# Kernel optimization log

Hardware: AMD Instinct MI355X
Metric: run time of the kernel (lower is better)

Reference implementation:

```python
import jax, jax.numpy as jnp
import numpy as np

B, S, D, H = 2, 2048, 256, 8
W_STD = 0.02


def setup_inputs() -> dict:
    key = jax.random.key(0)
    ks = jax.random.split(key, 6)
    x = jax.random.normal(ks[0], (B, S, D), jnp.float32)
    e = jax.random.normal(ks[1], (B, S, D), jnp.float32)
    p = jax.random.normal(ks[2], (B, S, D), jnp.float32)
    W_q = W_STD * jax.random.normal(ks[3], (D, D), jnp.float32)
    W_k = W_STD * jax.random.normal(ks[4], (D, D), jnp.float32)
    W_v = W_STD * jax.random.normal(ks[5], (D, D), jnp.float32)
    gamma = jnp.ones((H, 1, 1), jnp.float32)
    return {"x": x, "e": e, "p": p, "W_q": W_q, "W_k": W_k, "W_v": W_v, "gamma": gamma}


def reference(x, e, p, W_q, W_k, W_v, gamma):
    # use_ppe=True: Q = K = p (broadcast to every head), V = e; each head sees
    # the SAME d_embed-wide copy, so project once and broadcast over heads.
    Q = p @ W_q  # [B,S,D]
    K = p @ W_k  # [B,S,D]
    V = e @ W_v  # [B,S,D]
    # squared euclidean distance (torch.cdist(...,p=2)**2), shared across heads
    q2 = jnp.sum(Q * Q, axis=-1)  # [B,S]
    k2 = jnp.sum(K * K, axis=-1)  # [B,S]
    d2 = q2[:, :, None] + k2[:, None, :] - 2.0 * jnp.einsum('bsd,btd->bst', Q, K)
    d2 = jnp.maximum(d2, 0.0)  # [B,S,S]
    # rbf kernel, per-head gamma: krn = exp(-d2 / (-2*gamma + 1e-6))
    krn = -d2[:, None, :, :] / (-2.0 * gamma + 1e-6)  # [B,H,S,S]
    causal = jnp.tril(jnp.ones((S, S), dtype=bool))  # True where attending allowed
    krn = jnp.where(causal, krn, -jnp.inf)
    krn = jnp.exp(krn)  # masked entries -> exp(-inf) = 0
    # dropout layers run in eval mode (identity)
    out = jnp.einsum('bhst,btd->bhsd', krn, V)  # [B,H,S,D]
    return out
```

## Files before the change

### kernel.cpp

```cpp
#include <hip/hip_runtime.h>
#include <hip/hip_bf16.h>


#define BB   2
#define SS   2048
#define DD   256
#define HH   8
#define BSR  (BB*SS)
#define TSPLIT 4

typedef __bf16 bf16_t;
typedef __bf16 bf16x8 __attribute__((ext_vector_type(8)));
typedef float  f32x4  __attribute__((ext_vector_type(4)));

static __device__ __forceinline__ f32x4 mfma16(bf16x8 a, bf16x8 b, f32x4 c) {
    return __builtin_amdgcn_mfma_f32_16x16x32_bf16(a, b, c, 0, 0, 0);
}

__global__ __launch_bounds__(256) void att_wtrans(
    const float* __restrict__ Wq, const float* __restrict__ Wk,
    const float* __restrict__ Wv,
    bf16_t* __restrict__ WFq_h, bf16_t* __restrict__ WFq_l,
    bf16_t* __restrict__ WFk_h, bf16_t* __restrict__ WFk_l,
    bf16_t* __restrict__ WFv, float* __restrict__ q2, float* __restrict__ k2)
{
    __shared__ float tT[64][68];
    const int tid = threadIdx.x;
    if (blockIdx.x == 48) {
        for (int i = tid; i < BSR; i += 256) { q2[i] = 0.f; k2[i] = 0.f; }
        return;
    }
    const int mat = blockIdx.x >> 4;
    const int tl  = blockIdx.x & 15;
    const int tr  = (tl >> 2) * 64, tc = (tl & 3) * 64;
    const float* W = (mat == 0) ? Wq : ((mat == 1) ? Wk : Wv);

#pragma unroll
    for (int i = 0; i < 4; ++i) {
        const int fidx = i * 256 + tid;
        const int r  = fidx >> 4;
        const int c4 = fidx & 15;
        const float4 v = *(const float4*)(W + (size_t)(tr + r) * DD + tc + c4 * 4);
        tT[c4 * 4 + 0][r] = v.x; tT[c4 * 4 + 1][r] = v.y;
        tT[c4 * 4 + 2][r] = v.z; tT[c4 * 4 + 3][r] = v.w;
    }
    __syncthreads();

#pragma unroll
    for (int i = 0; i < 2; ++i) {
        const int uidx  = i * 256 + tid;
        const int chunk = uidx >> 6;
        const int kc_l  = chunk >> 2, c16 = chunk & 3;
        const int u = uidx & 63, m16 = u & 15, quad = u >> 4;
        const float* src = &tT[c16 * 16 + m16][kc_l * 32 + quad * 8];
        const float4 a = *(const float4*)src;
        const float4 bq = *(const float4*)(src + 4);
        const float f[8] = {a.x, a.y, a.z, a.w, bq.x, bq.y, bq.z, bq.w};
        bf16x8 hi, lo;
#pragma unroll
        for (int j = 0; j < 8; ++j) {
            const bf16_t h = (bf16_t)f[j];
            hi[j] = h; lo[j] = (bf16_t)(f[j] - (float)h);
        }
        const int g16 = (tc >> 4) + c16;
        const int kcg = (tr >> 5) + kc_l;
        const size_t off = ((size_t)(g16 * 8 + kcg)) * 512 + (size_t)u * 8;
        if (mat == 0)      { *(bf16x8*)(WFq_h + off) = hi; *(bf16x8*)(WFq_l + off) = lo; }
        else if (mat == 1) { *(bf16x8*)(WFk_h + off) = hi; *(bf16x8*)(WFk_l + off) = lo; }
        else               { *(bf16x8*)(WFv + off)  = hi; }
    }
}

__global__ __launch_bounds__(256) void att_zero_reps(
    const float* __restrict__ gamma, float* __restrict__ out)
{
    const int h = blockIdx.y & (HH - 1);
    const int b = blockIdx.y / HH;
    int rep = 0;
    while (gamma[rep] != gamma[h]) ++rep;
    if (rep != h) return;
    float4* dst = (float4*)(out + ((size_t)b * HH + h) * SS * DD);
    const int n4 = SS * DD / 4;
    for (int i = blockIdx.x * 256 + threadIdx.x; i < n4; i += 64 * 256)
        dst[i] = float4{0.f, 0.f, 0.f, 0.f};
}

__global__ __launch_bounds__(256, 2) void att_gemm_qkv(
    const float* __restrict__ p, const float* __restrict__ e,
    const bf16_t* __restrict__ WFq_h, const bf16_t* __restrict__ WFq_l,
    const bf16_t* __restrict__ WFk_h, const bf16_t* __restrict__ WFk_l,
    const bf16_t* __restrict__ WFv,
    bf16_t* __restrict__ Qh, bf16_t* __restrict__ Ql,
    bf16_t* __restrict__ Kh, bf16_t* __restrict__ Kl,
    bf16_t* __restrict__ Vt, float* __restrict__ q2, float* __restrict__ k2)
{
    __shared__ float pL[16][264];
    __shared__ float eL[16][264];
    __shared__ bf16_t vts[64][16];

    const int tid  = threadIdx.x;
    const int w    = tid >> 6;
    const int lane = tid & 63;
    const int m16  = lane & 15;
    const int quad = lane >> 4;
    const int row0 = (blockIdx.x >> 2) * 16;
    const int nb   = blockIdx.x & 3;
    const int ncol = nb * 64 + w * 16 + m16;

#pragma unroll
    for (int i = 0; i < 4; ++i) {
        const int fidx = i * 256 + tid;
        const int r  = fidx >> 6;
        const int c4 = fidx & 63;
        const float4 pv = *(const float4*)(p + (size_t)(row0 + r) * DD + c4 * 4);
        const float4 ev = *(const float4*)(e + (size_t)(row0 + r) * DD + c4 * 4);
        *(float4*)&pL[r][c4 * 4] = pv;
        *(float4*)&eL[r][c4 * 4] = ev;
    }
    __syncthreads();

    f32x4 aQ = f32x4{0.f, 0.f, 0.f, 0.f};
    f32x4 aK = f32x4{0.f, 0.f, 0.f, 0.f};
    f32x4 aV = f32x4{0.f, 0.f, 0.f, 0.f};

#pragma unroll 2
    for (int kc = 0; kc < 8; ++kc) {
        const float* ps = &pL[m16][kc * 32 + quad * 8];
        const float* es = &eL[m16][kc * 32 + quad * 8];
        const float4 p0 = *(const float4*)ps;
        const float4 p1 = *(const float4*)(ps + 4);
        const float4 e0 = *(const float4*)es;
        const float4 e1 = *(const float4*)(es + 4);
        const float pa[8] = {p0.x, p0.y, p0.z, p0.w, p1.x, p1.y, p1.z, p1.w};
        const float ea[8] = {e0.x, e0.y, e0.z, e0.w, e1.x, e1.y, e1.z, e1.w};
        bf16x8 aph, apl, aeb;
#pragma unroll
        for (int j = 0; j < 8; ++j) {
            const bf16_t h = (bf16_t)pa[j];
            aph[j] = h;
            apl[j] = (bf16_t)(pa[j] - (float)h);
            aeb[j] = (bf16_t)ea[j];
        }
        const size_t wo = ((size_t)((nb * 4 + w) * 8 + kc)) * 512 + (size_t)lane * 8;
        const bf16x8 bqh = *(const bf16x8*)(WFq_h + wo);
        const bf16x8 bql = *(const bf16x8*)(WFq_l + wo);
        const bf16x8 bkh = *(const bf16x8*)(WFk_h + wo);
        const bf16x8 bkl = *(const bf16x8*)(WFk_l + wo);
        const bf16x8 bv  = *(const bf16x8*)(WFv + wo);
        aQ = mfma16(aph, bqh, aQ);
        aQ = mfma16(apl, bqh, aQ);
        aQ = mfma16(aph, bql, aQ);
        aK = mfma16(aph, bkh, aK);
        aK = mfma16(apl, bkh, aK);
        aK = mfma16(aph, bkl, aK);
        aV = mfma16(aeb, bv, aV);
    }

    float sq[4], sk[4];
#pragma unroll
    for (int r = 0; r < 4; ++r) {
        const int rl = quad * 4 + r;
        const size_t go = (size_t)(row0 + rl) * DD + ncol;
        const float qv = aQ[r], kv = aK[r], vv = aV[r];
        const bf16_t qh_ = (bf16_t)qv; const bf16_t ql_ = (bf16_t)(qv - (float)qh_);
        const bf16_t kh_ = (bf16_t)kv; const bf16_t kl_ = (bf16_t)(kv - (float)kh_);
        Qh[go] = qh_; Ql[go] = ql_;
        Kh[go] = kh_; Kl[go] = kl_;
        sq[r] = qv * qv; sk[r] = kv * kv;
        vts[w * 16 + m16][rl] = (bf16_t)vv;
    }

#pragma unroll
    for (int r = 0; r < 4; ++r) {
        float vq = sq[r], vk = sk[r];
#pragma unroll
        for (int off = 8; off >= 1; off >>= 1) {
            vq += __shfl_xor(vq, off);
            vk += __shfl_xor(vk, off);
        }
        if (m16 == 0) {
            atomicAdd(q2 + row0 + quad * 4 + r, vq);
            atomicAdd(k2 + row0 + quad * 4 + r, vk);
        }
    }

    __syncthreads();
    if (tid < 64) {
        const int bb2 = row0 >> 11, t0v = row0 & 2047;
        bf16_t* dst = Vt + ((size_t)bb2 * DD + nb * 64 + tid) * SS + t0v;
        *(uint4*)dst       = *(const uint4*)&vts[tid][0];
        *((uint4*)dst + 1) = *(const uint4*)&vts[tid][8];
    }
}

__global__ __launch_bounds__(256) void att_repack(
    const bf16_t* __restrict__ Qh, const bf16_t* __restrict__ Ql,
    const bf16_t* __restrict__ Kh, const bf16_t* __restrict__ Kl,
    const bf16_t* __restrict__ Vt,
    bf16_t* __restrict__ QFh, bf16_t* __restrict__ QFl,
    bf16_t* __restrict__ KFh, bf16_t* __restrict__ KFl,
    bf16_t* __restrict__ VF)
{
    __shared__ bf16_t rowT[64][264];
    __shared__ bf16_t vT[256][72];

    const int tid  = threadIdx.x;
    const int tt   = blockIdx.x;
    const int part = blockIdx.y;
    const int b    = blockIdx.z;

    if (part < 4) {
        const bf16_t* src = (part == 0) ? Kh : (part == 1) ? Kl
                          : (part == 2) ? Qh : Ql;
#pragma unroll
        for (int i = 0; i < 8; ++i) {
            const int off = (i * 256 + tid) * 8;
            const int r = off >> 8, c = off & 255;
            *(bf16x8*)&rowT[r][c] =
                *(const bf16x8*)(src + ((size_t)(b * SS + tt * 64 + r)) * DD + c);
        }
        __syncthreads();
        if (part < 2) {
            bf16_t* dst = (part == 0) ? KFh : KFl;
#pragma unroll
            for (int i = 0; i < 8; ++i) {
                const int g = i * 256 + tid;
                const int chunk = g >> 6, u = g & 63;
                const int w_ = chunk >> 3, kc = chunk & 7;
                const bf16x8 v = *(const bf16x8*)
                    &rowT[w_ * 16 + (u & 15)][kc * 32 + (u >> 4) * 8];
                *(bf16x8*)(dst + ((size_t)(b * 32 + tt)) * 16384 + (size_t)g * 8) = v;
            }
        } else {
            bf16_t* dst = (part == 2) ? QFh : QFl;
#pragma unroll
            for (int i = 0; i < 8; ++i) {
                const int g = i * 256 + tid;
                const int chunk = g >> 6, u = g & 63;
                const int sub = chunk >> 4, mt = (chunk >> 3) & 1, kc = chunk & 7;
                const bf16x8 v = *(const bf16x8*)
                    &rowT[sub * 32 + mt * 16 + (u & 15)][kc * 32 + (u >> 4) * 8];
                const int st = tt * 2 + sub;
                *(bf16x8*)(dst + ((size_t)(b * 64 + st)) * 8192
                               + (size_t)(mt * 8 + kc) * 512 + (size_t)u * 8) = v;
            }
        }
    } else {
#pragma unroll
        for (int i = 0; i < 8; ++i) {
            const int off = (i * 256 + tid) * 8;
            const int d = off >> 6, tcol = off & 63;
            *(bf16x8*)&vT[d][tcol] =
                *(const bf16x8*)(Vt + ((size_t)(b * DD + d)) * SS + tt * 64 + tcol);
        }
        __syncthreads();
#pragma unroll
        for (int i = 0; i < 8; ++i) {
            const int g = i * 256 + tid;
            const int chunk = g >> 6, u = g & 63;
            const int w_ = chunk >> 3, kc2 = (chunk >> 2) & 1, nt = chunk & 3;
            const bf16x8 v = *(const bf16x8*)
                &vT[w_ * 64 + nt * 16 + (u & 15)][kc2 * 32 + (u >> 4) * 8];
            *(bf16x8*)(VF + ((size_t)(b * 32 + tt)) * 16384 + (size_t)g * 8) = v;
        }
    }
}

__global__ __launch_bounds__(256, 2) void att_flash(
    const bf16_t* __restrict__ QFh, const bf16_t* __restrict__ QFl,
    const bf16_t* __restrict__ KFh, const bf16_t* __restrict__ KFl,
    const bf16_t* __restrict__ VF, const float* __restrict__ q2,
    const float* __restrict__ k2, const float* __restrict__ gamma,
    float* __restrict__ out)
{
    __shared__ bf16_t Pb[2][32][72];

    const int tid   = threadIdx.x;
    const int pair  = blockIdx.x;
    const int split = blockIdx.y;
    const int b     = blockIdx.z;
    const int wave  = tid >> 6;
    const int lane  = tid & 63;
    const int m16   = lane & 15;
    const int quad  = lane >> 4;

    float g[8];
#pragma unroll
    for (int h = 0; h < 8; ++h) g[h] = gamma[h];

    int pb = 0;

    for (int half = 0; half < 2; ++half) {
        const int st = half ? (63 - pair) : pair;
        const int s0 = st * 32;

        bf16x8 aQh[2][8], aQl[2][8];
        const size_t qtile = ((size_t)(b * 64 + st)) * 8192 + (size_t)lane * 8;
#pragma unroll
        for (int mt = 0; mt < 2; ++mt)
#pragma unroll
            for (int kc = 0; kc < 8; ++kc) {
                const size_t base = qtile + (size_t)(mt * 8 + kc) * 512;
                aQh[mt][kc] = *(const bf16x8*)(QFh + base);
                aQl[mt][kc] = *(const bf16x8*)(QFl + base);
            }

        float q2r[2][4];
#pragma unroll
        for (int mt = 0; mt < 2; ++mt)
#pragma unroll
            for (int r = 0; r < 4; ++r)
                q2r[mt][r] = q2[b * SS + s0 + mt * 16 + quad * 4 + r];

        const int n_tiles = (s0 + 31) / 64 + 1;

        for (int h = 0; h < HH; ++h) {
            int rep = 0;
            while (g[rep] != g[h]) ++rep;
            if (rep != h) continue;
            const float cexp = 1.0f / (2.0f * g[h] - 1e-6f);

            f32x4 O[2][4];
#pragma unroll
            for (int mt = 0; mt < 2; ++mt)
#pragma unroll
                for (int nt = 0; nt < 4; ++nt)
                    O[mt][nt] = f32x4{0.f, 0.f, 0.f, 0.f};

            for (int ti = split; ti < n_tiles; ti += TSPLIT) {
                const int t0 = ti * 64;
                const int tg = t0 + wave * 16 + m16;
                const size_t tile = ((size_t)(b * 32 + ti)) * 16384
                                  + (size_t)wave * 4096 + (size_t)lane * 8;

                bf16x8 vf[2][4];
#pragma unroll
                for (int kc2 = 0; kc2 < 2; ++kc2)
#pragma unroll
                    for (int nt = 0; nt < 4; ++nt)
                        vf[kc2][nt] = *(const bf16x8*)(
                            VF + tile + (size_t)(kc2 * 4 + nt) * 512);
                const float k2v = k2[b * SS + tg];

                f32x4 acc0 = f32x4{0.f, 0.f, 0.f, 0.f};
                f32x4 acc1 = f32x4{0.f, 0.f, 0.f, 0.f};
#pragma unroll
                for (int kc = 0; kc < 8; ++kc) {
                    const bf16x8 bh = *(const bf16x8*)(KFh + tile + (size_t)kc * 512);
                    const bf16x8 bl = *(const bf16x8*)(KFl + tile + (size_t)kc * 512);
                    acc0 = mfma16(aQh[0][kc], bh, acc0);
                    acc1 = mfma16(aQh[1][kc], bh, acc1);
                    acc0 = mfma16(aQl[0][kc], bh, acc0);
                    acc1 = mfma16(aQl[1][kc], bh, acc1);
                    acc0 = mfma16(aQh[0][kc], bl, acc0);
                    acc1 = mfma16(aQh[1][kc], bl, acc1);
                }

#pragma unroll
                for (int mt = 0; mt < 2; ++mt) {
#pragma unroll
                    for (int r = 0; r < 4; ++r) {
                        const int sl = mt * 16 + quad * 4 + r;
                        const int sg = s0 + sl;
                        const float dotv = mt ? acc1[r] : acc0[r];
                        float d2 = q2r[mt][r] + k2v - 2.0f * dotv;
                        d2 = fmaxf(d2, 0.0f);
                        const float wgt = (tg <= sg) ? __expf(cexp * d2) : 0.0f;
                        Pb[pb][sl][wave * 16 + m16] = (bf16_t)wgt;
                    }
                }
                __syncthreads();

#pragma unroll
                for (int kc2 = 0; kc2 < 2; ++kc2) {
                    const bf16x8 pa0 = *(const bf16x8*)&Pb[pb][m16][kc2 * 32 + quad * 8];
                    const bf16x8 pa1 = *(const bf16x8*)&Pb[pb][m16 + 16][kc2 * 32 + quad * 8];
#pragma unroll
                    for (int nt = 0; nt < 4; ++nt) {
                        O[0][nt] = mfma16(pa0, vf[kc2][nt], O[0][nt]);
                        O[1][nt] = mfma16(pa1, vf[kc2][nt], O[1][nt]);
                    }
                }
                pb ^= 1;
            }

#pragma unroll
            for (int mt = 0; mt < 2; ++mt)
#pragma unroll
                for (int nt = 0; nt < 4; ++nt)
#pragma unroll
                    for (int r = 0; r < 4; ++r) {
                        const int sl   = mt * 16 + quad * 4 + r;
                        const int dcol = wave * 64 + nt * 16 + m16;
                        atomicAdd(out + (((size_t)b * HH + h) * SS + (s0 + sl)) * DD + dcol,
                                  O[mt][nt][r]);
                    }
        }
    }
}

__global__ __launch_bounds__(256) void att_copy_heads(
    const float* __restrict__ gamma, float* __restrict__ out)
{
    const int j = blockIdx.x * 256 + threadIdx.x;
    const int b = blockIdx.y;
    float4* o4 = (float4*)out + (size_t)b * HH * (SS * DD / 4);

    float g[8];
#pragma unroll
    for (int h = 0; h < 8; ++h) g[h] = gamma[h];

    float4 cached; int cached_rep = -1;
#pragma unroll
    for (int h = 1; h < HH; ++h) {
        int rep = 0;
        while (g[rep] != g[h]) ++rep;
        if (rep == h) continue;
        if (rep != cached_rep) {
            cached = o4[(size_t)rep * (SS * DD / 4) + j];
            cached_rep = rep;
        }
        o4[(size_t)h * (SS * DD / 4) + j] = cached;
    }
}

extern "C" void kernel_launch(void* const* d_in, const int* in_sizes, int n_in,
                              void* d_out, int out_size, void* d_ws, size_t ws_size,
                              hipStream_t stream) {
    (void)in_sizes; (void)n_in; (void)out_size; (void)ws_size;
    const float* e     = (const float*)d_in[1];
    const float* p     = (const float*)d_in[2];
    const float* Wq    = (const float*)d_in[3];
    const float* Wk    = (const float*)d_in[4];
    const float* Wv    = (const float*)d_in[5];
    const float* gamma = (const float*)d_in[6];

    const size_t NROW = (size_t)BSR * DD;
    bf16_t* Qh = (bf16_t*)d_ws;
    bf16_t* Ql = Qh + NROW;
    bf16_t* Kh = Ql + NROW;
    bf16_t* Kl = Kh + NROW;
    bf16_t* Vt = Kl + NROW;
    float*  q2 = (float*)(Vt + NROW);
    float*  k2 = q2 + BSR;
    bf16_t* WFq_h = (bf16_t*)(k2 + BSR);
    bf16_t* WFq_l = WFq_h + DD * DD;
    bf16_t* WFk_h = WFq_l + DD * DD;
    bf16_t* WFk_l = WFk_h + DD * DD;
    bf16_t* WFv   = WFk_l + DD * DD;
    bf16_t* QFh   = WFv + DD * DD;
    bf16_t* QFl   = QFh + NROW;
    bf16_t* KFh   = QFl + NROW;
    bf16_t* KFl   = KFh + NROW;
    bf16_t* VF    = KFl + NROW;

    float* out = (float*)d_out;

    att_wtrans<<<dim3(49), dim3(256), 0, stream>>>(
        Wq, Wk, Wv, WFq_h, WFq_l, WFk_h, WFk_l, WFv, q2, k2);

    att_zero_reps<<<dim3(64, BB * HH), dim3(256), 0, stream>>>(gamma, out);

    att_gemm_qkv<<<dim3((BSR / 16) * 4), dim3(256), 0, stream>>>(
        p, e, WFq_h, WFq_l, WFk_h, WFk_l, WFv, Qh, Ql, Kh, Kl, Vt, q2, k2);

    att_repack<<<dim3(32, 5, BB), dim3(256), 0, stream>>>(
        Qh, Ql, Kh, Kl, Vt, QFh, QFl, KFh, KFl, VF);

    att_flash<<<dim3(32, TSPLIT, BB), dim3(256), 0, stream>>>(
        QFh, QFl, KFh, KFl, VF, q2, k2, gamma, out);

    att_copy_heads<<<dim3(SS * DD / 4 / 256, BB), dim3(256), 0, stream>>>(
        gamma, out);
}
```

Before: 150.1 us.

## Fuse repack into QKV GEMM and replace atomic split-K with partial buffers

The QKV projection kernel now writes Q/K hi-lo and V directly in the MFMA fragment layout through shared-memory staging, so the separate repack kernel and its intermediate buffers go away. The flash kernel no longer does atomicAdd into a zeroed output. Split 0 stores to the output and splits 1-3 store to a partial workspace, and a single reduce-and-broadcast kernel sums them and copies to duplicate heads. The grid is also flattened so neighbouring blocks interleave splits and batches. This removes two launches, the zero-fill pass and the atomic traffic, at the cost of extra partial-buffer memory and read bandwidth in the final reduce.

```diff
diff --git a/kernel.cpp b/kernel.cpp
--- a/kernel.cpp
+++ b/kernel.cpp
@@ -71,32 +71,20 @@
     }
 }
 
-__global__ __launch_bounds__(256) void att_zero_reps(
-    const float* __restrict__ gamma, float* __restrict__ out)
-{
-    const int h = blockIdx.y & (HH - 1);
-    const int b = blockIdx.y / HH;
-    int rep = 0;
-    while (gamma[rep] != gamma[h]) ++rep;
-    if (rep != h) return;
-    float4* dst = (float4*)(out + ((size_t)b * HH + h) * SS * DD);
-    const int n4 = SS * DD / 4;
-    for (int i = blockIdx.x * 256 + threadIdx.x; i < n4; i += 64 * 256)
-        dst[i] = float4{0.f, 0.f, 0.f, 0.f};
-}
-
 __global__ __launch_bounds__(256, 2) void att_gemm_qkv(
     const float* __restrict__ p, const float* __restrict__ e,
     const bf16_t* __restrict__ WFq_h, const bf16_t* __restrict__ WFq_l,
     const bf16_t* __restrict__ WFk_h, const bf16_t* __restrict__ WFk_l,
     const bf16_t* __restrict__ WFv,
-    bf16_t* __restrict__ Qh, bf16_t* __restrict__ Ql,
-    bf16_t* __restrict__ Kh, bf16_t* __restrict__ Kl,
-    bf16_t* __restrict__ Vt, float* __restrict__ q2, float* __restrict__ k2)
+    bf16_t* __restrict__ QFh, bf16_t* __restrict__ QFl,
+    bf16_t* __restrict__ KFh, bf16_t* __restrict__ KFl,
+    bf16_t* __restrict__ VF, float* __restrict__ q2, float* __restrict__ k2)
 {
     __shared__ float pL[16][264];
     __shared__ float eL[16][264];
-    __shared__ bf16_t vts[64][16];
+    __shared__ float fQ[16][68];
+    __shared__ float fK[16][68];
+    __shared__ float fV[16][68];
 
     const int tid  = threadIdx.x;
     const int w    = tid >> 6;
@@ -105,7 +93,6 @@
     const int quad = lane >> 4;
     const int row0 = (blockIdx.x >> 2) * 16;
     const int nb   = blockIdx.x & 3;
-    const int ncol = nb * 64 + w * 16 + m16;
 
 #pragma unroll
     for (int i = 0; i < 4; ++i) {
@@ -156,23 +143,17 @@
         aV = mfma16(aeb, bv, aV);
     }
 
-    float sq[4], sk[4];
 #pragma unroll
     for (int r = 0; r < 4; ++r) {
         const int rl = quad * 4 + r;
-        const size_t go = (size_t)(row0 + rl) * DD + ncol;
-        const float qv = aQ[r], kv = aK[r], vv = aV[r];
-        const bf16_t qh_ = (bf16_t)qv; const bf16_t ql_ = (bf16_t)(qv - (float)qh_);
-        const bf16_t kh_ = (bf16_t)kv; const bf16_t kl_ = (bf16_t)(kv - (float)kh_);
-        Qh[go] = qh_; Ql[go] = ql_;
-        Kh[go] = kh_; Kl[go] = kl_;
-        sq[r] = qv * qv; sk[r] = kv * kv;
-        vts[w * 16 + m16][rl] = (bf16_t)vv;
+        fQ[rl][w * 16 + m16] = aQ[r];
+        fK[rl][w * 16 + m16] = aK[r];
+        fV[rl][w * 16 + m16] = aV[r];
     }
 
 #pragma unroll
     for (int r = 0; r < 4; ++r) {
-        float vq = sq[r], vk = sk[r];
+        float vq = aQ[r] * aQ[r], vk = aK[r] * aK[r];
 #pragma unroll
         for (int off = 8; off >= 1; off >>= 1) {
             vq += __shfl_xor(vq, off);
@@ -185,84 +166,59 @@
     }
 
     __syncthreads();
-    if (tid < 64) {
-        const int bb2 = row0 >> 11, t0v = row0 & 2047;
-        bf16_t* dst = Vt + ((size_t)bb2 * DD + nb * 64 + tid) * SS + t0v;
-        *(uint4*)dst       = *(const uint4*)&vts[tid][0];
-        *((uint4*)dst + 1) = *(const uint4*)&vts[tid][8];
-    }
-}
-
-__global__ __launch_bounds__(256) void att_repack(
-    const bf16_t* __restrict__ Qh, const bf16_t* __restrict__ Ql,
-    const bf16_t* __restrict__ Kh, const bf16_t* __restrict__ Kl,
-    const bf16_t* __restrict__ Vt,
-    bf16_t* __restrict__ QFh, bf16_t* __restrict__ QFl,
-    bf16_t* __restrict__ KFh, bf16_t* __restrict__ KFl,
-    bf16_t* __restrict__ VF)
-{
-    __shared__ bf16_t rowT[64][264];
-    __shared__ bf16_t vT[256][72];
-
-    const int tid  = threadIdx.x;
-    const int tt   = blockIdx.x;
-    const int part = blockIdx.y;
-    const int b    = blockIdx.z;
-
-    if (part < 4) {
-        const bf16_t* src = (part == 0) ? Kh : (part == 1) ? Kl
-                          : (part == 2) ? Qh : Ql;
-#pragma unroll
-        for (int i = 0; i < 8; ++i) {
-            const int off = (i * 256 + tid) * 8;
-            const int r = off >> 8, c = off & 255;
-            *(bf16x8*)&rowT[r][c] =
-                *(const bf16x8*)(src + ((size_t)(b * SS + tt * 64 + r)) * DD + c);
-        }
-        __syncthreads();
-        if (part < 2) {
-            bf16_t* dst = (part == 0) ? KFh : KFl;
-#pragma unroll
-            for (int i = 0; i < 8; ++i) {
-                const int g = i * 256 + tid;
-                const int chunk = g >> 6, u = g & 63;
-                const int w_ = chunk >> 3, kc = chunk & 7;
-                const bf16x8 v = *(const bf16x8*)
-                    &rowT[w_ * 16 + (u & 15)][kc * 32 + (u >> 4) * 8];
-                *(bf16x8*)(dst + ((size_t)(b * 32 + tt)) * 16384 + (size_t)g * 8) = v;
-            }
-        } else {
-            bf16_t* dst = (part == 2) ? QFh : QFl;
-#pragma unroll
-            for (int i = 0; i < 8; ++i) {
-                const int g = i * 256 + tid;
-                const int chunk = g >> 6, u = g & 63;
-                const int sub = chunk >> 4, mt = (chunk >> 3) & 1, kc = chunk & 7;
-                const bf16x8 v = *(const bf16x8*)
-                    &rowT[sub * 32 + mt * 16 + (u & 15)][kc * 32 + (u >> 4) * 8];
-                const int st = tt * 2 + sub;
-                *(bf16x8*)(dst + ((size_t)(b * 64 + st)) * 8192
-                               + (size_t)(mt * 8 + kc) * 512 + (size_t)u * 8) = v;
-            }
-        }
+
+    const int b   = row0 >> 11;
+    const int sl  = row0 & 2047;
+    const int tt  = sl >> 6;
+    const int st  = sl >> 5;
+    const int w4  = (sl >> 4) & 3;
+    const int mt  = (sl >> 4) & 1;
+    const int kc2 = (sl >> 5) & 1;
+    const int uh  = (sl >> 4) & 1;
+
+    if (w < 2) {
+        const int cl = w;
+        const float* src = &fQ[m16][cl * 32 + quad * 8];
+        const float4 a = *(const float4*)src;
+        const float4 c = *(const float4*)(src + 4);
+        const float f[8] = {a.x, a.y, a.z, a.w, c.x, c.y, c.z, c.w};
+        bf16x8 hi, lo;
+#pragma unroll
+        for (int j = 0; j < 8; ++j) {
+            const bf16_t h = (bf16_t)f[j];
+            hi[j] = h; lo[j] = (bf16_t)(f[j] - (float)h);
+        }
+        const size_t off = ((size_t)(b * 64 + st)) * 8192
+                         + (size_t)(mt * 8 + nb * 2 + cl) * 512 + (size_t)lane * 8;
+        *(bf16x8*)(QFh + off) = hi; *(bf16x8*)(QFl + off) = lo;
     } else {
-#pragma unroll
-        for (int i = 0; i < 8; ++i) {
-            const int off = (i * 256 + tid) * 8;
-            const int d = off >> 6, tcol = off & 63;
-            *(bf16x8*)&vT[d][tcol] =
-                *(const bf16x8*)(Vt + ((size_t)(b * DD + d)) * SS + tt * 64 + tcol);
-        }
-        __syncthreads();
-#pragma unroll
-        for (int i = 0; i < 8; ++i) {
-            const int g = i * 256 + tid;
-            const int chunk = g >> 6, u = g & 63;
-            const int w_ = chunk >> 3, kc2 = (chunk >> 2) & 1, nt = chunk & 3;
-            const bf16x8 v = *(const bf16x8*)
-                &vT[w_ * 64 + nt * 16 + (u & 15)][kc2 * 32 + (u >> 4) * 8];
-            *(bf16x8*)(VF + ((size_t)(b * 32 + tt)) * 16384 + (size_t)g * 8) = v;
-        }
+        const int cl = w - 2;
+        const float* src = &fK[m16][cl * 32 + quad * 8];
+        const float4 a = *(const float4*)src;
+        const float4 c = *(const float4*)(src + 4);
+        const float f[8] = {a.x, a.y, a.z, a.w, c.x, c.y, c.z, c.w};
+        bf16x8 hi, lo;
+#pragma unroll
+        for (int j = 0; j < 8; ++j) {
+            const bf16_t h = (bf16_t)f[j];
+            hi[j] = h; lo[j] = (bf16_t)(f[j] - (float)h);
+        }
+        const size_t off = ((size_t)(b * 32 + tt)) * 16384
+                         + (size_t)(w4 * 8 + nb * 2 + cl) * 512 + (size_t)lane * 8;
+        *(bf16x8*)(KFh + off) = hi; *(bf16x8*)(KFl + off) = lo;
+    }
+
+    if (lane < 32) {
+        const int nt  = w;
+        const int u   = uh * 32 + lane;
+        const int tl0 = (lane >> 4) * 8;
+        bf16x8 vb;
+#pragma unroll
+        for (int j = 0; j < 8; ++j)
+            vb[j] = (bf16_t)fV[tl0 + j][nt * 16 + (lane & 15)];
+        const size_t off = ((size_t)(b * 32 + tt)) * 16384
+                         + (size_t)(nb * 8 + kc2 * 4 + nt) * 512 + (size_t)u * 8;
+        *(bf16x8*)(VF + off) = vb;
     }
 }
 
@@ -271,14 +227,15 @@
     const bf16_t* __restrict__ KFh, const bf16_t* __restrict__ KFl,
     const bf16_t* __restrict__ VF, const float* __restrict__ q2,
     const float* __restrict__ k2, const float* __restrict__ gamma,
-    float* __restrict__ out)
+    float* __restrict__ part, float* __restrict__ out)
 {
     __shared__ bf16_t Pb[2][32][72];
 
     const int tid   = threadIdx.x;
-    const int pair  = blockIdx.x;
-    const int split = blockIdx.y;
-    const int b     = blockIdx.z;
+    const int pair  = blockIdx.x >> 3;
+    const int sub   = blockIdx.x & 7;
+    const int split = sub >> 1;
+    const int b     = sub & 1;
     const int wave  = tid >> 6;
     const int lane  = tid & 63;
     const int m16   = lane & 15;
@@ -384,43 +341,58 @@
                 pb ^= 1;
             }
 
+            float* dst = (split == 0)
+                ? out  + (((size_t)b * HH + h) * SS + s0) * DD
+                : part + ((((size_t)(split - 1) * BB + b) * HH + h) * SS + s0) * DD;
 #pragma unroll
             for (int mt = 0; mt < 2; ++mt)
 #pragma unroll
                 for (int nt = 0; nt < 4; ++nt)
 #pragma unroll
-                    for (int r = 0; r < 4; ++r) {
-                        const int sl   = mt * 16 + quad * 4 + r;
-                        const int dcol = wave * 64 + nt * 16 + m16;
-                        atomicAdd(out + (((size_t)b * HH + h) * SS + (s0 + sl)) * DD + dcol,
-                                  O[mt][nt][r]);
-                    }
-        }
-    }
-}
-
-__global__ __launch_bounds__(256) void att_copy_heads(
-    const float* __restrict__ gamma, float* __restrict__ out)
+                    for (int r = 0; r < 4; ++r)
+                        dst[(size_t)(mt * 16 + quad * 4 + r) * DD
+                            + wave * 64 + nt * 16 + m16] = O[mt][nt][r];
+        }
+    }
+}
+
+__global__ __launch_bounds__(256) void att_reduce_bcast(
+    const float* __restrict__ gamma, const float* __restrict__ part,
+    float* __restrict__ out)
 {
     const int j = blockIdx.x * 256 + threadIdx.x;
     const int b = blockIdx.y;
-    float4* o4 = (float4*)out + (size_t)b * HH * (SS * DD / 4);
+    const int slab = SS * DD / 4;
 
     float g[8];
 #pragma unroll
     for (int h = 0; h < 8; ++h) g[h] = gamma[h];
 
-    float4 cached; int cached_rep = -1;
-#pragma unroll
-    for (int h = 1; h < HH; ++h) {
+    const float4* pp = (const float4*)part;
+    float4* o4 = (float4*)out;
+
+    float4 repval{0.f, 0.f, 0.f, 0.f};
+    int last_rep = -1;
+#pragma unroll
+    for (int h = 0; h < HH; ++h) {
         int rep = 0;
         while (g[rep] != g[h]) ++rep;
-        if (rep == h) continue;
-        if (rep != cached_rep) {
-            cached = o4[(size_t)rep * (SS * DD / 4) + j];
-            cached_rep = rep;
-        }
-        o4[(size_t)h * (SS * DD / 4) + j] = cached;
+        float4* o = o4 + ((size_t)(b * HH + h)) * slab + j;
+        if (rep == h) {
+            float4 v = *o;
+#pragma unroll
+            for (int k = 0; k < 3; ++k) {
+                const float4 pv = pp[(((size_t)k * BB + b) * HH + h) * slab + j];
+                v.x += pv.x; v.y += pv.y; v.z += pv.z; v.w += pv.w;
+            }
+            *o = v; repval = v; last_rep = h;
+        } else {
+            if (last_rep != rep) {
+                repval = o4[((size_t)(b * HH + rep)) * slab + j];
+                last_rep = rep;
+            }
+            *o = repval;
+        }
     }
 }
 
@@ -436,40 +408,31 @@
     const float* gamma = (const float*)d_in[6];
 
     const size_t NROW = (size_t)BSR * DD;
-    bf16_t* Qh = (bf16_t*)d_ws;
-    bf16_t* Ql = Qh + NROW;
-    bf16_t* Kh = Ql + NROW;
-    bf16_t* Kl = Kh + NROW;
-    bf16_t* Vt = Kl + NROW;
-    float*  q2 = (float*)(Vt + NROW);
-    float*  k2 = q2 + BSR;
-    bf16_t* WFq_h = (bf16_t*)(k2 + BSR);
+    bf16_t* WFq_h = (bf16_t*)d_ws;
     bf16_t* WFq_l = WFq_h + DD * DD;
     bf16_t* WFk_h = WFq_l + DD * DD;
     bf16_t* WFk_l = WFk_h + DD * DD;
     bf16_t* WFv   = WFk_l + DD * DD;
-    bf16_t* QFh   = WFv + DD * DD;
+    float*  q2    = (float*)(WFv + DD * DD);
+    float*  k2    = q2 + BSR;
+    bf16_t* QFh   = (bf16_t*)(k2 + BSR);
     bf16_t* QFl   = QFh + NROW;
     bf16_t* KFh   = QFl + NROW;
     bf16_t* KFl   = KFh + NROW;
     bf16_t* VF    = KFl + NROW;
+    float*  part  = (float*)(VF + NROW);
 
     float* out = (float*)d_out;
 
     att_wtrans<<<dim3(49), dim3(256), 0, stream>>>(
         Wq, Wk, Wv, WFq_h, WFq_l, WFk_h, WFk_l, WFv, q2, k2);
 
-    att_zero_reps<<<dim3(64, BB * HH), dim3(256), 0, stream>>>(gamma, out);
-
     att_gemm_qkv<<<dim3((BSR / 16) * 4), dim3(256), 0, stream>>>(
-        p, e, WFq_h, WFq_l, WFk_h, WFk_l, WFv, Qh, Ql, Kh, Kl, Vt, q2, k2);
-
-    att_repack<<<dim3(32, 5, BB), dim3(256), 0, stream>>>(
-        Qh, Ql, Kh, Kl, Vt, QFh, QFl, KFh, KFl, VF);
-
-    att_flash<<<dim3(32, TSPLIT, BB), dim3(256), 0, stream>>>(
-        QFh, QFl, KFh, KFl, VF, q2, k2, gamma, out);
-
-    att_copy_heads<<<dim3(SS * DD / 4 / 256, BB), dim3(256), 0, stream>>>(
-        gamma, out);
-}
+        p, e, WFq_h, WFq_l, WFk_h, WFk_l, WFv, QFh, QFl, KFh, KFl, VF, q2, k2);
+
+    att_flash<<<dim3(32 * TSPLIT * BB), dim3(256), 0, stream>>>(
+        QFh, QFl, KFh, KFl, VF, q2, k2, gamma, part, out);
+
+    att_reduce_bcast<<<dim3(SS * DD / 4 / 256, BB), dim3(256), 0, stream>>>(
+        gamma, part, out);
+}
```

Result: faster. 136.1 us (-9.4%).
